# Kernel optimization log

Hardware: AMD Instinct MI355X
Metric: run time of the kernel (lower is better)

The kernel has to match this reference:

```python
import jax, jax.numpy as jnp
import numpy as np

K = 3  # kernel_size
S = 1  # stride
P = 1  # padding


def setup_inputs() -> dict:
    key = jax.random.key(0)
    ks = jax.random.split(key, 5)
    B, C, H, W, O = 4, 64, 128, 128, 64
    x = jax.random.normal(ks[0], (B, C, H, W), jnp.float32)
    # offset conv params (module inits these to 0; use small random values so the
    # bilinear-gather path is actually exercised with non-integer offsets)
    w_off = jax.random.normal(ks[1], (2 * K * K, C, K, K), jnp.float32) * 0.01
    b_off = jax.random.normal(ks[2], (2 * K * K,), jnp.float32) * 0.01
    # deformable conv params (torchvision DeformConv2d has bias=True by default)
    w_dcn = jax.random.normal(ks[3], (O, C, K, K), jnp.float32) * (1.0 / np.sqrt(C * K * K))
    b_dcn = jax.random.normal(ks[4], (O,), jnp.float32) * 0.01
    return {"x": x, "w_off": w_off, "b_off": b_off, "w_dcn": w_dcn, "b_dcn": b_dcn}


def _conv(x, w, b):
    y = jax.lax.conv_general_dilated(
        x, w, window_strides=(S, S), padding=[(P, P), (P, P)],
        dimension_numbers=("NCHW", "OIHW", "NCHW"))
    return y + b[None, :, None, None]


def _deform_conv2d(x, offset, w_dcn, b_dcn):
    # x: [B,C,H,W]; offset: [B, 2*K*K, Ho, Wo] with (dy, dx) interleaved per
    # kernel tap (row-major kh*K+kw), matching torchvision deform_conv2d.
    B, C, H, W = x.shape
    Ho, Wo = offset.shape[2], offset.shape[3]
    K2 = K * K
    off = offset.reshape(B, K2, 2, Ho, Wo)
    oy, ox = off[:, :, 0], off[:, :, 1]  # [B,K2,Ho,Wo]

    kh = (jnp.arange(K2) // K).astype(jnp.float32)
    kw = (jnp.arange(K2) % K).astype(jnp.float32)
    base_y = (jnp.arange(Ho) * S - P).astype(jnp.float32)
    base_x = (jnp.arange(Wo) * S - P).astype(jnp.float32)
    # fractional sampling locations: p0 + p_k + offset
    py = base_y[None, None, :, None] + kh[None, :, None, None] + oy  # [B,K2,Ho,Wo]
    px = base_x[None, None, None, :] + kw[None, :, None, None] + ox

    y0f = jnp.floor(py); x0f = jnp.floor(px)
    dy = py - y0f; dx = px - x0f
    y0 = y0f.astype(jnp.int32); x0 = x0f.astype(jnp.int32)

    def gather(yi, xi):
        # implicit zero padding: mask out-of-range corners
        valid = (yi >= 0) & (yi < H) & (xi >= 0) & (xi < W)
        yc = jnp.clip(yi, 0, H - 1)
        xc = jnp.clip(xi, 0, W - 1)
        v = jax.vmap(lambda xb, yb, xib: xb[:, yb, xib])(x, yc, xc)  # [B,C,K2,Ho,Wo]
        return v * valid[:, None].astype(x.dtype)

    v00 = gather(y0, x0)
    v01 = gather(y0, x0 + 1)
    v10 = gather(y0 + 1, x0)
    v11 = gather(y0 + 1, x0 + 1)

    wy = dy[:, None]; wx = dx[:, None]  # [B,1,K2,Ho,Wo]
    sampled = (v00 * (1 - wy) * (1 - wx) + v01 * (1 - wy) * wx
               + v10 * wy * (1 - wx) + v11 * wy * wx)  # [B,C,K2,Ho,Wo]

    O = w_dcn.shape[0]
    out = jnp.einsum("bckij,ock->boij", sampled, w_dcn.reshape(O, C, K2))
    return out + b_dcn[None, :, None, None]


def reference(x, w_off, b_off, w_dcn, b_dcn):
    offset = _conv(x, w_off, b_off)          # [B, 2*K*K, Ho, Wo]
    return _deform_conv2d(x, offset, w_dcn, b_dcn)
```

## Files before the change

### kernel.cpp

```cpp
#include <hip/hip_runtime.h>
#include <hip/hip_fp16.h>

#define B_ 4
#define H_ 128
#define W_ 128
#define HW_ 16384

typedef _Float16 half8 __attribute__((ext_vector_type(8)));
typedef float floatx4 __attribute__((ext_vector_type(4)));


__global__ __launch_bounds__(256) void k_prep(
    const float* __restrict__ x, const float* __restrict__ w_dcn,
    const float* __restrict__ w_off,
    __half* __restrict__ W2L, __half* __restrict__ W0L,
    _Float16* __restrict__ xh)
{
    int bid = blockIdx.x;
    int t = threadIdx.x;
    if (bid < 2048) {
        int idx = bid*256 + t;
        int p  = idx & (HW_-1);
        int bc = idx >> 14;
        const float* s = x + (size_t)bc*8*HW_ + p;
        half8 vv;
        #pragma unroll
        for (int e = 0; e < 8; ++e) vv[e] = (_Float16)s[e*HW_];
        *(half8*)(xh + (size_t)idx*8) = vv;
    } else {
        int idx = (bid - 2048)*256 + t;
        if (idx < 36864) {
            int e = idx & 7, lane = (idx>>3) & 63, og = (idx>>9) & 3;
            int ks = (idx>>11) & 1, tap = idx >> 12;
            int o = og*16 + (lane & 15);
            int c = ks*32 + ((lane >> 4) & 3)*8 + e;
            W2L[idx] = __float2half(w_dcn[o*576 + c*9 + tap]);
        } else {
            int i2 = idx - 36864;
            int e = i2 & 7, lane = (i2>>3) & 63, og = (i2>>9) & 1;
            int ks = (i2>>10) & 1, tap = i2 >> 11;
            int oc = og*16 + (lane & 15);
            int c = ks*32 + ((lane >> 4) & 3)*8 + e;
            W0L[i2] = (oc < 18) ? __float2half(w_off[oc*576 + c*9 + tap])
                                : __float2half(0.f);
        }
    }
}

#define DESC_STRIDE 2304
#define E_OFF 9216
#define SMEM_SZ 26368

__global__ __launch_bounds__(256, 4) void k_fused(
    const _Float16* __restrict__ xh,
    const _Float16* __restrict__ W2L, const _Float16* __restrict__ W0L,
    const float* __restrict__ b_off, const float* __restrict__ b_dcn,
    float* __restrict__ out)
{
    __shared__ __attribute__((aligned(16))) char smem[SMEM_SZ];

    int t = threadIdx.x;
    int lane = t & 63;
    int w = __builtin_amdgcn_readfirstlane(t >> 6);
    int c15 = lane & 15;
    int q   = (lane >> 4) & 3;

    char*  wreg = smem + w*DESC_STRIDE;
    float* offL = (float*)wreg;
    char*  desc = wreg;

    int bid  = blockIdx.x;
    int xcd  = bid & 7, sidx = bid >> 3;
    int orig = xcd*128 + sidx;
    int b    = orig >> 8;
    int rem  = orig & 255;
    int i    = rem >> 1;
    int j0b  = (rem & 1) * 64;
    int j0   = j0b + w*16;

    const _Float16* xq0 = xh + (((size_t)(b*8) + q    ) << 17);
    const _Float16* xq1 = xh + (((size_t)(b*8) + 4 + q) << 17);

    floatx4 accA0 = {0.f,0.f,0.f,0.f};
    floatx4 accA1 = accA0;
    const half8 hz = {0,0,0,0,0,0,0,0};
    #pragma unroll 3
    for (int tap = 0; tap < 9; ++tap) {
        int kh = tap/3, kw = tap - (tap/3)*3;
        int py = i - 1 + kh;
        int px = j0 + c15 - 1 + kw;
        bool valid = (py >= 0) && (py < H_) && (px >= 0) && (px < W_);
        int pyc = min(max(py, 0), H_-1);
        int pxc = min(max(px, 0), W_-1);
        int pix = (pyc << 7) + pxc;
        #pragma unroll
        for (int ks = 0; ks < 2; ++ks) {
            const _Float16* xq = ks ? xq1 : xq0;
            half8 a = *(const half8*)(xq + (size_t)pix*8);
            a = valid ? a : hz;
            half8 bf0 = *(const half8*)(W0L + ((tap*4 + ks*2 + 0)<<9) + (lane<<3));
            half8 bf1 = *(const half8*)(W0L + ((tap*4 + ks*2 + 1)<<9) + (lane<<3));
            accA0 = __builtin_amdgcn_mfma_f32_16x16x32_f16(a, bf0, accA0, 0, 0, 0);
            accA1 = __builtin_amdgcn_mfma_f32_16x16x32_f16(a, bf1, accA1, 0, 0, 0);
        }
    }
    {
        float bo0 = b_off[c15];
        #pragma unroll
        for (int r = 0; r < 4; ++r) {
            int pos = q*4 + r;
            offL[pos*18 + c15] = accA0[r] + bo0;
        }
        int oc1 = 16 + c15;
        if (oc1 < 18) {
            float bo1 = b_off[oc1];
            #pragma unroll
            for (int r = 0; r < 4; ++r) {
                int pos = q*4 + r;
                offL[pos*18 + oc1] = accA1[r] + bo1;
            }
        }
    }

    float2 o2r[3];
    #pragma unroll
    for (int e = 0; e < 3; ++e) {
        int idx = e*64 + lane;
        if (idx < 144) {
            int pl = idx / 9, tap = idx - pl*9;
            o2r[e] = *(const float2*)(offL + pl*18 + 2*tap);
        }
    }
    uint4 dreg[3];
    #pragma unroll
    for (int e = 0; e < 3; ++e) {
        int idx = e*64 + lane;
        if (idx < 144) {
            int pl = idx / 9, tap = idx - pl*9;
            int kh = tap/3, kw = tap - (tap/3)*3;
            float py = (float)(i - 1 + kh) + o2r[e].x;
            float px = (float)(j0 + pl - 1 + kw) + o2r[e].y;
            float y0f = floorf(py), x0f = floorf(px);
            float dy = py - y0f, dx = px - x0f;
            int y0 = (int)y0f, x0i = (int)x0f;
            int y1 = y0 + 1,  x1 = x0i + 1;
            bool vy0 = (y0>=0)&(y0<H_),   vy1 = (y1>=0)&(y1<H_);
            bool vx0 = (x0i>=0)&(x0i<W_), vx1 = (x1>=0)&(x1<W_);
            int yc0 = min(max(y0,0),H_-1),  yc1 = min(max(y1,0),H_-1);
            int xc0 = min(max(x0i,0),W_-1), xc1 = min(max(x1,0),W_-1);
            float w00 = (1.f-dy)*(1.f-dx) * ((vy0&&vx0)?1.f:0.f);
            float w01 = (1.f-dy)*dx       * ((vy0&&vx1)?1.f:0.f);
            float w10 = dy*(1.f-dx)       * ((vy1&&vx0)?1.f:0.f);
            float w11 = dy*dx             * ((vy1&&vx1)?1.f:0.f);
            unsigned a0 = (yc0<<7)+xc0, a1 = (yc0<<7)+xc1;
            unsigned a2 = (yc1<<7)+xc0, a3 = (yc1<<7)+xc1;
            __half2 hw0 = __floats2half2_rn(w00, w01);
            __half2 hw1 = __floats2half2_rn(w10, w11);
            dreg[e].x = a0 | (a1 << 16);
            dreg[e].y = a2 | (a3 << 16);
            dreg[e].z = *(unsigned*)&hw0;
            dreg[e].w = *(unsigned*)&hw1;
        }
    }
    #pragma unroll
    for (int e = 0; e < 3; ++e) {
        int idx = e*64 + lane;
        if (idx < 144) {
            int pl = idx / 9, tap = idx - pl*9;
            *(uint4*)(desc + (pl*9 + tap)*16) = dreg[e];
        }
    }

    floatx4 acc0 = {0.f,0.f,0.f,0.f};
    floatx4 acc1 = acc0, acc2 = acc0, acc3 = acc0;

    #pragma unroll 3
    for (int tap = 0; tap < 9; ++tap) {
        uint4 d = *(const uint4*)(desc + (c15*9 + tap)*16);
        unsigned p0 = d.x & 0xffffu, p1 = d.x >> 16;
        unsigned p2 = d.y & 0xffffu, p3 = d.y >> 16;
        unsigned short b00 = (unsigned short)(d.z & 0xffffu);
        unsigned short b01 = (unsigned short)(d.z >> 16);
        unsigned short b10 = (unsigned short)(d.w & 0xffffu);
        unsigned short b11 = (unsigned short)(d.w >> 16);
        _Float16 h00 = *(_Float16*)&b00, h01 = *(_Float16*)&b01;
        _Float16 h10 = *(_Float16*)&b10, h11 = *(_Float16*)&b11;
        half8 W00 = {h00,h00,h00,h00,h00,h00,h00,h00};
        half8 W01 = {h01,h01,h01,h01,h01,h01,h01,h01};
        half8 W10 = {h10,h10,h10,h10,h10,h10,h10,h10};
        half8 W11 = {h11,h11,h11,h11,h11,h11,h11,h11};
        #pragma unroll
        for (int s = 0; s < 2; ++s) {
            const _Float16* xq = s ? xq1 : xq0;
            half8 v00 = *(const half8*)(xq + (size_t)p0*8);
            half8 v01 = *(const half8*)(xq + (size_t)p1*8);
            half8 v10 = *(const half8*)(xq + (size_t)p2*8);
            half8 v11 = *(const half8*)(xq + (size_t)p3*8);
            half8 sk = v00*W00 + v01*W01 + v10*W10 + v11*W11;
            half8 bfa = *(const half8*)(W2L + ((tap*8 + s*4 + 0)<<9) + (lane<<3));
            acc0 = __builtin_amdgcn_mfma_f32_16x16x32_f16(sk, bfa, acc0, 0, 0, 0);
            half8 bfb = *(const half8*)(W2L + ((tap*8 + s*4 + 1)<<9) + (lane<<3));
            acc1 = __builtin_amdgcn_mfma_f32_16x16x32_f16(sk, bfb, acc1, 0, 0, 0);
            half8 bfc = *(const half8*)(W2L + ((tap*8 + s*4 + 2)<<9) + (lane<<3));
            acc2 = __builtin_amdgcn_mfma_f32_16x16x32_f16(sk, bfc, acc2, 0, 0, 0);
            half8 bfd = *(const half8*)(W2L + ((tap*8 + s*4 + 3)<<9) + (lane<<3));
            acc3 = __builtin_amdgcn_mfma_f32_16x16x32_f16(sk, bfd, acc3, 0, 0, 0);
        }
    }

    float* E = (float*)(smem + E_OFF);
    #pragma unroll
    for (int r = 0; r < 4; ++r) {
        int pl = w*16 + q*4 + r;
        E[pl*67 + c15]      = acc0[r];
        E[pl*67 + 16 + c15] = acc1[r];
        E[pl*67 + 32 + c15] = acc2[r];
        E[pl*67 + 48 + c15] = acc3[r];
    }
    __syncthreads();
    int obase = (b*64)*HW_ + i*W_ + j0b;
    #pragma unroll
    for (int rep = 0; rep < 16; ++rep) {
        int o = rep*4 + w;
        out[obase + o*HW_ + lane] = E[lane*67 + o] + b_dcn[o];
    }
}

extern "C" void kernel_launch(void* const* d_in, const int* in_sizes, int n_in,
                              void* d_out, int out_size, void* d_ws, size_t ws_size,
                              hipStream_t stream) {
    const float* x     = (const float*)d_in[0];
    const float* w_off = (const float*)d_in[1];
    const float* b_off = (const float*)d_in[2];
    const float* w_dcn = (const float*)d_in[3];
    const float* b_dcn = (const float*)d_in[4];
    float* out = (float*)d_out;

    __half* W2L = (__half*)d_ws;
    __half* W0L = (__half*)((char*)d_ws + 73728);
    _Float16* xh = (_Float16*)((char*)d_ws + 110592);

    k_prep<<<2264, 256, 0, stream>>>(x, w_dcn, w_off, W2L, W0L, xh);
    k_fused<<<1024, 256, 0, stream>>>((const _Float16*)xh, (const _Float16*)W2L,
                                      (const _Float16*)W0L, b_off, b_dcn, out);
}
```

Baseline: 109.6 us.

## Stage 2x32 tile input halo in LDS via direct global-to-LDS loads

Each block now covers a 2-row by 32-column output tile instead of a 1x64 row strip. Before any compute, it copies a 6x36 fp16 halo of all 64 channels into shared memory with global_load_lds. Both the offset-conv taps and the bilinear gathers then read from LDS, and only samples whose offsets land outside the halo fall back to global memory, flagged by a bit in the descriptor. This is meant to cut repeated scattered global/L2 reads of the same neighbourhood. The cost is a larger LDS footprint, which may lower occupancy, plus an extra barrier and a divergent fallback path.

```diff
diff --git a/kernel.cpp b/kernel.cpp
--- a/kernel.cpp
+++ b/kernel.cpp
@@ -8,6 +8,8 @@
 
 typedef _Float16 half8 __attribute__((ext_vector_type(8)));
 typedef float floatx4 __attribute__((ext_vector_type(4)));
+typedef __attribute__((address_space(3))) void lds_void;
+typedef const __attribute__((address_space(1))) void gbl_void;
 
 
 __global__ __launch_bounds__(256) void k_prep(
@@ -47,9 +49,10 @@
     }
 }
 
+#define CHS2 3456
+#define DESC_OFF 27648
 #define DESC_STRIDE 2304
-#define E_OFF 9216
-#define SMEM_SZ 26368
+#define SMEM_SZ 36864
 
 __global__ __launch_bounds__(256, 4) void k_fused(
     const _Float16* __restrict__ xh,
@@ -58,14 +61,17 @@
     float* __restrict__ out)
 {
     __shared__ __attribute__((aligned(16))) char smem[SMEM_SZ];
+    char* halo_c = smem;
 
     int t = threadIdx.x;
     int lane = t & 63;
     int w = __builtin_amdgcn_readfirstlane(t >> 6);
+    int rw = w & 1;
+    int cw = (w >> 1) * 16;
     int c15 = lane & 15;
     int q   = (lane >> 4) & 3;
 
-    char*  wreg = smem + w*DESC_STRIDE;
+    char*  wreg = smem + DESC_OFF + w*DESC_STRIDE;
     float* offL = (float*)wreg;
     char*  desc = wreg;
 
@@ -74,12 +80,26 @@
     int orig = xcd*128 + sidx;
     int b    = orig >> 8;
     int rem  = orig & 255;
-    int i    = rem >> 1;
-    int j0b  = (rem & 1) * 64;
-    int j0   = j0b + w*16;
-
-    const _Float16* xq0 = xh + (((size_t)(b*8) + q    ) << 17);
-    const _Float16* xq1 = xh + (((size_t)(b*8) + 4 + q) << 17);
+    int i0   = (rem >> 2) * 2;
+    int j0   = (rem & 3) * 32;
+
+    {
+        const _Float16* xhb = xh + ((size_t)b << 20);
+        for (int i = w; i < 27; i += 4) {
+            int idx = (i << 6) + lane;
+            int ch  = idx / 216;
+            int pl  = idx - ch*216;
+            int hr  = pl / 36;
+            int hx  = pl - hr*36;
+            int grow = min(max(i0 - 2 + hr, 0), H_-1);
+            int gcol = min(max(j0 - 2 + hx, 0), W_-1);
+            const _Float16* g = xhb + ((size_t)ch << 17) + (size_t)(((grow<<7) + gcol) << 3);
+            __builtin_amdgcn_global_load_lds((gbl_void*)g,
+                                             (lds_void*)(halo_c + (i << 10)),
+                                             16, 0, 0);
+        }
+    }
+    __syncthreads();
 
     floatx4 accA0 = {0.f,0.f,0.f,0.f};
     floatx4 accA1 = accA0;
@@ -87,16 +107,13 @@
     #pragma unroll 3
     for (int tap = 0; tap < 9; ++tap) {
         int kh = tap/3, kw = tap - (tap/3)*3;
-        int py = i - 1 + kh;
-        int px = j0 + c15 - 1 + kw;
+        int py = i0 + rw - 1 + kh;
+        int px = j0 + cw + c15 - 1 + kw;
         bool valid = (py >= 0) && (py < H_) && (px >= 0) && (px < W_);
-        int pyc = min(max(py, 0), H_-1);
-        int pxc = min(max(px, 0), W_-1);
-        int pix = (pyc << 7) + pxc;
+        int pixA = (rw + 1 + kh)*36 + (cw + c15 + 1 + kw);
         #pragma unroll
         for (int ks = 0; ks < 2; ++ks) {
-            const _Float16* xq = ks ? xq1 : xq0;
-            half8 a = *(const half8*)(xq + (size_t)pix*8);
+            half8 a = *(const half8*)(halo_c + (ks*4 + q)*CHS2 + pixA*16);
             a = valid ? a : hz;
             half8 bf0 = *(const half8*)(W0L + ((tap*4 + ks*2 + 0)<<9) + (lane<<3));
             half8 bf1 = *(const half8*)(W0L + ((tap*4 + ks*2 + 1)<<9) + (lane<<3));
@@ -107,18 +124,14 @@
     {
         float bo0 = b_off[c15];
         #pragma unroll
-        for (int r = 0; r < 4; ++r) {
-            int pos = q*4 + r;
-            offL[pos*18 + c15] = accA0[r] + bo0;
-        }
+        for (int r = 0; r < 4; ++r)
+            offL[(q*4 + r)*18 + c15] = accA0[r] + bo0;
         int oc1 = 16 + c15;
         if (oc1 < 18) {
             float bo1 = b_off[oc1];
             #pragma unroll
-            for (int r = 0; r < 4; ++r) {
-                int pos = q*4 + r;
-                offL[pos*18 + oc1] = accA1[r] + bo1;
-            }
+            for (int r = 0; r < 4; ++r)
+                offL[(q*4 + r)*18 + oc1] = accA1[r] + bo1;
         }
     }
 
@@ -138,8 +151,8 @@
         if (idx < 144) {
             int pl = idx / 9, tap = idx - pl*9;
             int kh = tap/3, kw = tap - (tap/3)*3;
-            float py = (float)(i - 1 + kh) + o2r[e].x;
-            float px = (float)(j0 + pl - 1 + kw) + o2r[e].y;
+            float py = (float)(i0 + rw - 1 + kh) + o2r[e].x;
+            float px = (float)(j0 + cw + pl - 1 + kw) + o2r[e].y;
             float y0f = floorf(py), x0f = floorf(px);
             float dy = py - y0f, dx = px - x0f;
             int y0 = (int)y0f, x0i = (int)x0f;
@@ -152,8 +165,14 @@
             float w01 = (1.f-dy)*dx       * ((vy0&&vx1)?1.f:0.f);
             float w10 = dy*(1.f-dx)       * ((vy1&&vx0)?1.f:0.f);
             float w11 = dy*dx             * ((vy1&&vx1)?1.f:0.f);
-            unsigned a0 = (yc0<<7)+xc0, a1 = (yc0<<7)+xc1;
-            unsigned a2 = (yc1<<7)+xc0, a3 = (yc1<<7)+xc1;
+            int hy0 = yc0 - (i0-2), hy1 = yc1 - (i0-2);
+            int hx0 = xc0 - (j0-2), hx1 = xc1 - (j0-2);
+            bool inh = ((unsigned)hy0 < 6u) & ((unsigned)hy1 < 6u)
+                     & ((unsigned)hx0 < 36u) & ((unsigned)hx1 < 36u);
+            unsigned a0,a1,a2,a3;
+            if (inh) { a0 = hy0*36+hx0; a1 = hy0*36+hx1; a2 = hy1*36+hx0; a3 = hy1*36+hx1; }
+            else     { a0 = ((yc0<<7)+xc0) | 0x8000u; a1 = (yc0<<7)+xc1;
+                       a2 = (yc1<<7)+xc0;             a3 = (yc1<<7)+xc1; }
             __half2 hw0 = __floats2half2_rn(w00, w01);
             __half2 hw1 = __floats2half2_rn(w10, w11);
             dreg[e].x = a0 | (a1 << 16);
@@ -174,11 +193,17 @@
     floatx4 acc0 = {0.f,0.f,0.f,0.f};
     floatx4 acc1 = acc0, acc2 = acc0, acc3 = acc0;
 
+    const char* hbA = halo_c + (0*4 + q)*CHS2;
+    const char* hbB = halo_c + (4 + q)*CHS2;
+    const _Float16* xqA = xh + (((size_t)(b*8) + q    ) << 17);
+    const _Float16* xqB = xh + (((size_t)(b*8) + 4 + q) << 17);
+
     #pragma unroll 3
     for (int tap = 0; tap < 9; ++tap) {
         uint4 d = *(const uint4*)(desc + (c15*9 + tap)*16);
-        unsigned p0 = d.x & 0xffffu, p1 = d.x >> 16;
+        unsigned p0 = d.x & 0x7fffu, p1 = d.x >> 16;
         unsigned p2 = d.y & 0xffffu, p3 = d.y >> 16;
+        bool inh = (d.x & 0x8000u) == 0u;
         unsigned short b00 = (unsigned short)(d.z & 0xffffu);
         unsigned short b01 = (unsigned short)(d.z >> 16);
         unsigned short b10 = (unsigned short)(d.w & 0xffffu);
@@ -189,40 +214,51 @@
         half8 W01 = {h01,h01,h01,h01,h01,h01,h01,h01};
         half8 W10 = {h10,h10,h10,h10,h10,h10,h10,h10};
         half8 W11 = {h11,h11,h11,h11,h11,h11,h11,h11};
-        #pragma unroll
-        for (int s = 0; s < 2; ++s) {
-            const _Float16* xq = s ? xq1 : xq0;
-            half8 v00 = *(const half8*)(xq + (size_t)p0*8);
-            half8 v01 = *(const half8*)(xq + (size_t)p1*8);
-            half8 v10 = *(const half8*)(xq + (size_t)p2*8);
-            half8 v11 = *(const half8*)(xq + (size_t)p3*8);
+        const char* hb[2] = {hbA, hbB};
+        const _Float16* xq[2] = {xqA, xqB};
+        #pragma unroll
+        for (int ks = 0; ks < 2; ++ks) {
+            half8 v00, v01, v10, v11;
+            if (inh) {
+                v00 = *(const half8*)(hb[ks] + p0*16);
+                v01 = *(const half8*)(hb[ks] + p1*16);
+                v10 = *(const half8*)(hb[ks] + p2*16);
+                v11 = *(const half8*)(hb[ks] + p3*16);
+            } else {
+                v00 = *(const half8*)(xq[ks] + (size_t)p0*8);
+                v01 = *(const half8*)(xq[ks] + (size_t)p1*8);
+                v10 = *(const half8*)(xq[ks] + (size_t)p2*8);
+                v11 = *(const half8*)(xq[ks] + (size_t)p3*8);
+            }
             half8 sk = v00*W00 + v01*W01 + v10*W10 + v11*W11;
-            half8 bfa = *(const half8*)(W2L + ((tap*8 + s*4 + 0)<<9) + (lane<<3));
+            half8 bfa = *(const half8*)(W2L + ((tap*8 + ks*4 + 0)<<9) + (lane<<3));
             acc0 = __builtin_amdgcn_mfma_f32_16x16x32_f16(sk, bfa, acc0, 0, 0, 0);
-            half8 bfb = *(const half8*)(W2L + ((tap*8 + s*4 + 1)<<9) + (lane<<3));
+            half8 bfb = *(const half8*)(W2L + ((tap*8 + ks*4 + 1)<<9) + (lane<<3));
             acc1 = __builtin_amdgcn_mfma_f32_16x16x32_f16(sk, bfb, acc1, 0, 0, 0);
-            half8 bfc = *(const half8*)(W2L + ((tap*8 + s*4 + 2)<<9) + (lane<<3));
+            half8 bfc = *(const half8*)(W2L + ((tap*8 + ks*4 + 2)<<9) + (lane<<3));
             acc2 = __builtin_amdgcn_mfma_f32_16x16x32_f16(sk, bfc, acc2, 0, 0, 0);
-            half8 bfd = *(const half8*)(W2L + ((tap*8 + s*4 + 3)<<9) + (lane<<3));
+            half8 bfd = *(const half8*)(W2L + ((tap*8 + ks*4 + 3)<<9) + (lane<<3));
             acc3 = __builtin_amdgcn_mfma_f32_16x16x32_f16(sk, bfd, acc3, 0, 0, 0);
         }
     }
-
-    float* E = (float*)(smem + E_OFF);
+    __syncthreads();
+
+    float* E = (float*)smem;
     #pragma unroll
     for (int r = 0; r < 4; ++r) {
-        int pl = w*16 + q*4 + r;
+        int pl = rw*32 + cw + q*4 + r;
         E[pl*67 + c15]      = acc0[r];
         E[pl*67 + 16 + c15] = acc1[r];
         E[pl*67 + 32 + c15] = acc2[r];
         E[pl*67 + 48 + c15] = acc3[r];
     }
     __syncthreads();
-    int obase = (b*64)*HW_ + i*W_ + j0b;
+    int obase = (b*64)*HW_ + i0*W_ + j0;
+    int prow = (lane >> 5)*W_ + (lane & 31);
     #pragma unroll
     for (int rep = 0; rep < 16; ++rep) {
         int o = rep*4 + w;
-        out[obase + o*HW_ + lane] = E[lane*67 + o] + b_dcn[o];
+        out[obase + o*HW_ + prow] = E[lane*67 + o] + b_dcn[o];
     }
 }
 
```

Result: faster. 103.2 us (-5.9%).
